# Kernel optimization log

Measured on AMD Instinct MI355X. Metric: run time of the kernel, lower is better.

The kernel has to match this reference:

```python
import jax, jax.numpy as jnp
import numpy as np

ENT_GRID = 16
ENT_DIM = 64
N_RELATION = 5000
EMB_DIM = ENT_GRID * ENT_DIM  # 1024
BATCH = 8192
LN_EPS = 1e-5


def setup_inputs() -> dict:
    key = jax.random.key(0)
    k1, k2, k3, k4 = jax.random.split(key, 4)
    ent_emb = jax.random.normal(k1, (BATCH, EMB_DIM), dtype=jnp.float32)
    proj_ids = jax.random.randint(k2, (BATCH,), 0, N_RELATION, dtype=jnp.int64)
    # xavier_uniform for relation_tran: fan_in = fan_out treated over last two dims
    lim_t = float(np.sqrt(6.0 / (ENT_GRID + ENT_GRID)))
    relation_tran = jax.random.uniform(
        k3, (N_RELATION, ENT_DIM, ENT_GRID, ENT_GRID), jnp.float32, -lim_t, lim_t)
    lim_b = float(np.sqrt(6.0 / (ENT_DIM + ENT_GRID)))
    relation_bias = jax.random.uniform(
        k4, (N_RELATION, ENT_DIM, ENT_GRID), jnp.float32, -lim_b, lim_b)
    ln_weight = jnp.ones((EMB_DIM,), dtype=jnp.float32)
    ln_bias = jnp.zeros((EMB_DIM,), dtype=jnp.float32)
    return {
        "ent_emb": ent_emb,
        "proj_ids": proj_ids,
        "relation_tran": relation_tran,
        "relation_bias": relation_bias,
        "ln_weight": ln_weight,
        "ln_bias": ln_bias,
    }


def _layer_norm(x, w, b, eps=LN_EPS):
    mu = jnp.mean(x, axis=-1, keepdims=True)
    var = jnp.mean(jnp.square(x - mu), axis=-1, keepdims=True)
    return (x - mu) * jax.lax.rsqrt(var + eps) * w + b


def reference(ent_emb, proj_ids, relation_tran, relation_bias, ln_weight, ln_bias):
    B = ent_emb.shape[0]
    # gather per-query relation transform and bias
    rel_tran = relation_tran[proj_ids]  # (B, ent_dim, g, g)
    rel_bias = relation_bias[proj_ids]  # (B, ent_dim, g)
    # distribute: (B, emb_dim) -> (B, ent_dim, ent_grid); torch.chunk+stack == contiguous reshape
    e = ent_emb.reshape(B, ENT_DIM, ENT_GRID)
    # batched small matmul: (g,g) @ (g,) per (batch, ent_dim) block, plus bias
    x = jnp.einsum('bdgh,bdh->bdg', rel_tran, e) + rel_bias
    out = _layer_norm(x.reshape(B, EMB_DIM), ln_weight, ln_bias)
    return out
```

## Files before the change

kernel.cpp:

```cpp
#include <hip/hip_runtime.h>

#define ENT_GRID 16
#define ENT_DIM  64
#define EMB      1024
#define LN_EPS   1e-5f


__global__ void zero_hist_kernel(int* __restrict__ hist, int n) {
    int i = blockIdx.x * blockDim.x + threadIdx.x;
    if (i < n) hist[i] = 0;
}

__global__ void hist_kernel(const int* __restrict__ ids, int* __restrict__ hist, int B) {
    int i = blockIdx.x * blockDim.x + threadIdx.x;
    if (i < B) atomicAdd(&hist[ids[i]], 1);
}

__global__ __launch_bounds__(1024)
void scan_kernel(const int* __restrict__ hist, int* __restrict__ cursor, int n) {
    const int t = threadIdx.x;
    const int ITEMS = (n + 1023) / 1024;
    int vals[8];
    int lsum = 0;
#pragma unroll
    for (int k = 0; k < 8; ++k) {
        int i = t * ITEMS + k;
        int v = (k < ITEMS && i < n) ? hist[i] : 0;
        vals[k] = v;
        lsum += v;
    }
    __shared__ int s[1024];
    s[t] = lsum;
    __syncthreads();
    for (int off = 1; off < 1024; off <<= 1) {
        int v = (t >= off) ? s[t - off] : 0;
        __syncthreads();
        s[t] += v;
        __syncthreads();
    }
    int run = s[t] - lsum;
#pragma unroll
    for (int k = 0; k < 8; ++k) {
        int i = t * ITEMS + k;
        if (k < ITEMS && i < n) cursor[i] = run;
        run += vals[k];
    }
}

__global__ void scatter_kernel(const int* __restrict__ ids, int* __restrict__ cursor,
                               int* __restrict__ perm, int B) {
    int i = blockIdx.x * blockDim.x + threadIdx.x;
    if (i < B) {
        int pos = atomicAdd(&cursor[ids[i]], 1);
        perm[pos] = i;
    }
}

__device__ __forceinline__ float dot4(float4 a, float4 b) {
    return a.x * b.x + a.y * b.y + a.z * b.z + a.w * b.w;
}

__global__ __launch_bounds__(1024, 8)
void wproj_group_kernel(const float* __restrict__ ent_emb,
                        const float* __restrict__ rel_tran,
                        const float* __restrict__ rel_bias,
                        const float* __restrict__ ln_w,
                        const float* __restrict__ ln_b,
                        const int*   __restrict__ hist,
                        const int*   __restrict__ cursor_end,
                        const int*   __restrict__ perm,
                        float* __restrict__ out) {
    const int r   = blockIdx.x;
    const int cnt = hist[r];
    if (cnt == 0) return;
    const int start = cursor_end[r] - cnt;
    const int t = threadIdx.x;
    const int w = t >> 6;

    const float4* __restrict__ tr4 = reinterpret_cast<const float4*>(
        rel_tran + (size_t)r * (ENT_DIM * ENT_GRID * ENT_GRID) + (size_t)t * ENT_GRID);
    const float4 t0 = tr4[0], t1 = tr4[1], t2 = tr4[2], t3 = tr4[3];
    const float bv  = rel_bias[(size_t)r * EMB + t];
    const float lwv = ln_w[t];
    const float lbv = ln_b[t];

    __shared__ __align__(16) float se[2][EMB];
    __shared__ __align__(16) float wred[2][2][16];

    int   bcur = perm[start];
    float vcur = ent_emb[(size_t)bcur * EMB + t];

    for (int j = 0; j < cnt; ++j) {
        const int jb = j & 1;
        se[jb][t] = vcur;

        int bnext = 0; float vnext = 0.0f;
        if (j + 1 < cnt) {
            bnext = perm[start + j + 1];
            vnext = ent_emb[(size_t)bnext * EMB + t];
        }

        asm volatile("s_waitcnt lgkmcnt(0)\n\ts_barrier" ::: "memory");

        const float4* __restrict__ er =
            reinterpret_cast<const float4*>(&se[jb][(t >> 4) * ENT_GRID]);
        const float x = bv + dot4(t0, er[0]) + dot4(t1, er[1])
                           + dot4(t2, er[2]) + dot4(t3, er[3]);

        float s = x, ss = x * x;
#pragma unroll
        for (int off = 32; off > 0; off >>= 1) {
            s  += __shfl_xor(s, off, 64);
            ss += __shfl_xor(ss, off, 64);
        }
        if ((t & 63) == 0) { wred[jb][0][w] = s; wred[jb][1][w] = ss; }

        asm volatile("s_waitcnt lgkmcnt(0)\n\ts_barrier" ::: "memory");

        float tsum = 0.0f, tsq = 0.0f;
        const float4* __restrict__ ps = reinterpret_cast<const float4*>(&wred[jb][0][0]);
        const float4* __restrict__ pq = reinterpret_cast<const float4*>(&wred[jb][1][0]);
#pragma unroll
        for (int q = 0; q < 4; ++q) {
            const float4 a = ps[q];
            const float4 c = pq[q];
            tsum += a.x + a.y + a.z + a.w;
            tsq  += c.x + c.y + c.z + c.w;
        }
        const float mu   = tsum * (1.0f / (float)EMB);
        const float var  = tsq * (1.0f / (float)EMB) - mu * mu;
        const float rstd = rsqrtf(var + LN_EPS);

        out[(size_t)bcur * EMB + t] = (x - mu) * rstd * lwv + lbv;

        bcur = bnext;
        vcur = vnext;
    }
}

extern "C" void kernel_launch(void* const* d_in, const int* in_sizes, int n_in,
                              void* d_out, int out_size, void* d_ws, size_t ws_size,
                              hipStream_t stream) {
    const float* ent_emb  = (const float*)d_in[0];
    const int*   proj_ids = (const int*)  d_in[1];
    const float* rel_tran = (const float*)d_in[2];
    const float* rel_bias = (const float*)d_in[3];
    const float* ln_w     = (const float*)d_in[4];
    const float* ln_b     = (const float*)d_in[5];
    float* out = (float*)d_out;

    const int B  = in_sizes[1];
    const int NR = in_sizes[2] / (ENT_DIM * ENT_GRID * ENT_GRID);

    int* w      = (int*)d_ws;
    int* hist   = w;
    int* cursor = w + NR;
    int* perm   = w + 2 * NR;

    zero_hist_kernel<<<(NR + 255) / 256, 256, 0, stream>>>(hist, NR);
    hist_kernel<<<(B + 255) / 256, 256, 0, stream>>>(proj_ids, hist, B);
    scan_kernel<<<1, 1024, 0, stream>>>(hist, cursor, NR);
    scatter_kernel<<<(B + 255) / 256, 256, 0, stream>>>(proj_ids, cursor, perm, B);

    wproj_group_kernel<<<NR, 1024, 0, stream>>>(ent_emb, rel_tran, rel_bias, ln_w, ln_b,
                                                hist, cursor, perm, out);
}
```

Before: 100.1 us.

## Split relation-grouped projection into quarter blocks and separate LayerNorm pass

The 1024-thread per-relation block becomes four 256-thread blocks, each covering a quarter of the embedding. Each block writes the unnormalized projection plus per-wave partial sums to workspace, and a new per-row kernel then reduces the partials and applies LayerNorm in place. This removes the two block-wide barriers per row and spreads relation work across more, smaller blocks. In exchange the output is written and read an extra time, each quarter reads the entity row from global memory directly, and there is one more launch.

```diff
diff --git a/kernel.cpp b/kernel.cpp
--- a/kernel.cpp
+++ b/kernel.cpp
@@ -60,52 +60,39 @@
     return a.x * b.x + a.y * b.y + a.z * b.z + a.w * b.w;
 }
 
-__global__ __launch_bounds__(1024, 8)
-void wproj_group_kernel(const float* __restrict__ ent_emb,
-                        const float* __restrict__ rel_tran,
-                        const float* __restrict__ rel_bias,
-                        const float* __restrict__ ln_w,
-                        const float* __restrict__ ln_b,
-                        const int*   __restrict__ hist,
-                        const int*   __restrict__ cursor_end,
-                        const int*   __restrict__ perm,
-                        float* __restrict__ out) {
-    const int r   = blockIdx.x;
+__global__ __launch_bounds__(256, 8)
+void wproj_quarter_kernel(const float* __restrict__ ent_emb,
+                          const float* __restrict__ rel_tran,
+                          const float* __restrict__ rel_bias,
+                          const int*   __restrict__ hist,
+                          const int*   __restrict__ cursor_end,
+                          const int*   __restrict__ perm,
+                          float* __restrict__ xout,
+                          float2* __restrict__ part) {
+    const int blk = blockIdx.x;
+    const int r   = blk >> 2;
+    const int q   = blk & 3;
     const int cnt = hist[r];
     if (cnt == 0) return;
     const int start = cursor_end[r] - cnt;
     const int t = threadIdx.x;
     const int w = t >> 6;
+    const int i = q * 256 + t;
+    const int d = i >> 4;
 
     const float4* __restrict__ tr4 = reinterpret_cast<const float4*>(
-        rel_tran + (size_t)r * (ENT_DIM * ENT_GRID * ENT_GRID) + (size_t)t * ENT_GRID);
-    const float4 t0 = tr4[0], t1 = tr4[1], t2 = tr4[2], t3 = tr4[3];
-    const float bv  = rel_bias[(size_t)r * EMB + t];
-    const float lwv = ln_w[t];
-    const float lbv = ln_b[t];
-
-    __shared__ __align__(16) float se[2][EMB];
-    __shared__ __align__(16) float wred[2][2][16];
-
-    int   bcur = perm[start];
-    float vcur = ent_emb[(size_t)bcur * EMB + t];
+        rel_tran + (size_t)r * (ENT_DIM * ENT_GRID * ENT_GRID) + (size_t)i * ENT_GRID);
+    const float4 a0 = tr4[0], a1 = tr4[1], a2 = tr4[2], a3 = tr4[3];
+    const float bv = rel_bias[(size_t)r * EMB + i];
 
     for (int j = 0; j < cnt; ++j) {
-        const int jb = j & 1;
-        se[jb][t] = vcur;
+        const int b = perm[start + j];
+        const float4* __restrict__ e4 =
+            reinterpret_cast<const float4*>(ent_emb + (size_t)b * EMB + d * ENT_GRID);
+        const float4 e0 = e4[0], e1 = e4[1], e2 = e4[2], e3 = e4[3];
 
-        int bnext = 0; float vnext = 0.0f;
-        if (j + 1 < cnt) {
-            bnext = perm[start + j + 1];
-            vnext = ent_emb[(size_t)bnext * EMB + t];
-        }
-
-        asm volatile("s_waitcnt lgkmcnt(0)\n\ts_barrier" ::: "memory");
-
-        const float4* __restrict__ er =
-            reinterpret_cast<const float4*>(&se[jb][(t >> 4) * ENT_GRID]);
-        const float x = bv + dot4(t0, er[0]) + dot4(t1, er[1])
-                           + dot4(t2, er[2]) + dot4(t3, er[3]);
+        const float x = bv + dot4(a0, e0) + dot4(a1, e1) + dot4(a2, e2) + dot4(a3, e3);
+        xout[(size_t)b * EMB + i] = x;
 
         float s = x, ss = x * x;
 #pragma unroll
@@ -113,29 +100,47 @@
             s  += __shfl_xor(s, off, 64);
             ss += __shfl_xor(ss, off, 64);
         }
-        if ((t & 63) == 0) { wred[jb][0][w] = s; wred[jb][1][w] = ss; }
+        if ((t & 63) == 0) part[(size_t)b * 16 + q * 4 + w] = make_float2(s, ss);
+    }
+}
 
-        asm volatile("s_waitcnt lgkmcnt(0)\n\ts_barrier" ::: "memory");
+__global__ __launch_bounds__(256, 8)
+void ln_kernel(const float2* __restrict__ part,
+               const float*  __restrict__ ln_w,
+               const float*  __restrict__ ln_b,
+               float* __restrict__ out) {
+    const int b = blockIdx.x;
+    const int t = threadIdx.x;
+    __shared__ float sstat[2];
 
-        float tsum = 0.0f, tsq = 0.0f;
-        const float4* __restrict__ ps = reinterpret_cast<const float4*>(&wred[jb][0][0]);
-        const float4* __restrict__ pq = reinterpret_cast<const float4*>(&wred[jb][1][0]);
+    if (t < 64) {
+        float s = 0.0f, ss = 0.0f;
+        if (t < 16) { const float2 p = part[(size_t)b * 16 + t]; s = p.x; ss = p.y; }
 #pragma unroll
-        for (int q = 0; q < 4; ++q) {
-            const float4 a = ps[q];
-            const float4 c = pq[q];
-            tsum += a.x + a.y + a.z + a.w;
-            tsq  += c.x + c.y + c.z + c.w;
+        for (int off = 8; off > 0; off >>= 1) {
+            s  += __shfl_xor(s, off, 64);
+            ss += __shfl_xor(ss, off, 64);
         }
-        const float mu   = tsum * (1.0f / (float)EMB);
-        const float var  = tsq * (1.0f / (float)EMB) - mu * mu;
-        const float rstd = rsqrtf(var + LN_EPS);
+        if (t == 0) {
+            const float mu  = s * (1.0f / (float)EMB);
+            const float var = ss * (1.0f / (float)EMB) - mu * mu;
+            sstat[0] = mu;
+            sstat[1] = rsqrtf(var + LN_EPS);
+        }
+    }
+    __syncthreads();
+    const float mu = sstat[0], rstd = sstat[1];
 
-        out[(size_t)bcur * EMB + t] = (x - mu) * rstd * lwv + lbv;
-
-        bcur = bnext;
-        vcur = vnext;
-    }
+    float4* __restrict__ o4 = reinterpret_cast<float4*>(out + (size_t)b * EMB);
+    const float4 x  = o4[t];
+    const float4 w  = reinterpret_cast<const float4*>(ln_w)[t];
+    const float4 bb = reinterpret_cast<const float4*>(ln_b)[t];
+    float4 o;
+    o.x = (x.x - mu) * rstd * w.x + bb.x;
+    o.y = (x.y - mu) * rstd * w.y + bb.y;
+    o.z = (x.z - mu) * rstd * w.z + bb.z;
+    o.w = (x.w - mu) * rstd * w.w + bb.w;
+    o4[t] = o;
 }
 
 extern "C" void kernel_launch(void* const* d_in, const int* in_sizes, int n_in,
@@ -156,12 +161,16 @@
     int* hist   = w;
     int* cursor = w + NR;
     int* perm   = w + 2 * NR;
+    size_t int_bytes = (size_t)(2 * NR + B) * sizeof(int);
+    int_bytes = (int_bytes + 15) & ~(size_t)15;
+    float2* part = (float2*)((char*)d_ws + int_bytes);
 
     zero_hist_kernel<<<(NR + 255) / 256, 256, 0, stream>>>(hist, NR);
     hist_kernel<<<(B + 255) / 256, 256, 0, stream>>>(proj_ids, hist, B);
     scan_kernel<<<1, 1024, 0, stream>>>(hist, cursor, NR);
     scatter_kernel<<<(B + 255) / 256, 256, 0, stream>>>(proj_ids, cursor, perm, B);
 
-    wproj_group_kernel<<<NR, 1024, 0, stream>>>(ent_emb, rel_tran, rel_bias, ln_w, ln_b,
-                                                hist, cursor, perm, out);
+    wproj_quarter_kernel<<<NR * 4, 256, 0, stream>>>(ent_emb, rel_tran, rel_bias,
+                                                     hist, cursor, perm, out, part);
+    ln_kernel<<<B, 256, 0, stream>>>(part, ln_w, ln_b, out);
 }
```

Measured after the change: 99.97 us. About the same (-0.1%).

## Compact nonempty relations into work list and compute four outputs per thread

Applied to the files above, without the earlier changes.

The scan kernel now emits a compacted list of nonempty relations (id, start, count), and the main kernel indexes that list instead of launching per-relation blocks that exit early. The main kernel drops to 256 threads, each holding a full 4x16 transform slice in registers and reading entity vectors directly from global memory as float4, which removes the shared-memory staging and one barrier per row. The zero kernel is replaced by a memset. This cuts empty-block overhead and synchronization, at the cost of much higher register pressure (64 floats of transform per thread) and redundant global reads of entity data across threads.

```diff
diff --git a/kernel.cpp b/kernel.cpp
--- a/kernel.cpp
+++ b/kernel.cpp
@@ -6,18 +6,14 @@
 #define LN_EPS   1e-5f
 
 
-__global__ void zero_hist_kernel(int* __restrict__ hist, int n) {
-    int i = blockIdx.x * blockDim.x + threadIdx.x;
-    if (i < n) hist[i] = 0;
-}
-
 __global__ void hist_kernel(const int* __restrict__ ids, int* __restrict__ hist, int B) {
     int i = blockIdx.x * blockDim.x + threadIdx.x;
     if (i < B) atomicAdd(&hist[ids[i]], 1);
 }
 
 __global__ __launch_bounds__(1024)
-void scan_kernel(const int* __restrict__ hist, int* __restrict__ cursor, int n) {
+void scan_kernel(const int* __restrict__ hist, int* __restrict__ cursor,
+                 int4* __restrict__ work, int* __restrict__ nwork, int n) {
     const int t = threadIdx.x;
     const int ITEMS = (n + 1023) / 1024;
     int vals[8];
@@ -42,7 +38,13 @@
 #pragma unroll
     for (int k = 0; k < 8; ++k) {
         int i = t * ITEMS + k;
-        if (k < ITEMS && i < n) cursor[i] = run;
+        if (k < ITEMS && i < n) {
+            cursor[i] = run;
+            if (vals[k] > 0) {
+                int idx = atomicAdd(nwork, 1);
+                work[idx] = make_int4(i, run, vals[k], 0);
+            }
+        }
         run += vals[k];
     }
 }
@@ -60,81 +62,92 @@
     return a.x * b.x + a.y * b.y + a.z * b.z + a.w * b.w;
 }
 
-__global__ __launch_bounds__(1024, 8)
-void wproj_group_kernel(const float* __restrict__ ent_emb,
+__global__ __launch_bounds__(256, 3)
+void wproj_fused_kernel(const float* __restrict__ ent_emb,
                         const float* __restrict__ rel_tran,
                         const float* __restrict__ rel_bias,
                         const float* __restrict__ ln_w,
                         const float* __restrict__ ln_b,
-                        const int*   __restrict__ hist,
-                        const int*   __restrict__ cursor_end,
+                        const int4*  __restrict__ work,
+                        const int*   __restrict__ nwork,
                         const int*   __restrict__ perm,
                         float* __restrict__ out) {
-    const int r   = blockIdx.x;
-    const int cnt = hist[r];
-    if (cnt == 0) return;
-    const int start = cursor_end[r] - cnt;
-    const int t = threadIdx.x;
-    const int w = t >> 6;
+    const int w = blockIdx.x;
+    if (w >= *nwork) return;
+    const int4 wk   = work[w];
+    const int r     = wk.x;
+    const int start = wk.y;
+    const int cnt   = wk.z;
+    const int t  = threadIdx.x;
+    const int wv = t >> 6;
+    const int d  = t >> 2;
 
     const float4* __restrict__ tr4 = reinterpret_cast<const float4*>(
-        rel_tran + (size_t)r * (ENT_DIM * ENT_GRID * ENT_GRID) + (size_t)t * ENT_GRID);
-    const float4 t0 = tr4[0], t1 = tr4[1], t2 = tr4[2], t3 = tr4[3];
-    const float bv  = rel_bias[(size_t)r * EMB + t];
-    const float lwv = ln_w[t];
-    const float lbv = ln_b[t];
+        rel_tran + (size_t)r * (ENT_DIM * ENT_GRID * ENT_GRID) + (size_t)t * 64);
+    float4 trv[16];
+#pragma unroll
+    for (int m = 0; m < 16; ++m) trv[m] = tr4[m];
+    const float4 bv = reinterpret_cast<const float4*>(rel_bias + (size_t)r * EMB)[t];
+    const float4 lw = reinterpret_cast<const float4*>(ln_w)[t];
+    const float4 lb = reinterpret_cast<const float4*>(ln_b)[t];
 
-    __shared__ __align__(16) float se[2][EMB];
-    __shared__ __align__(16) float wred[2][2][16];
+    __shared__ float2 wred[2][4];
 
-    int   bcur = perm[start];
-    float vcur = ent_emb[(size_t)bcur * EMB + t];
+    const int last = start + cnt - 1;
+    int b0 = perm[start];
+    int b1 = perm[min(start + 1, last)];
+    {
+        const float4* __restrict__ e4 =
+            reinterpret_cast<const float4*>(ent_emb + (size_t)b0 * EMB + d * ENT_GRID);
+        float4 e0 = e4[0], e1 = e4[1], e2 = e4[2], e3 = e4[3];
 
-    for (int j = 0; j < cnt; ++j) {
-        const int jb = j & 1;
-        se[jb][t] = vcur;
+        for (int j = 0; j < cnt; ++j) {
+            const int jb = j & 1;
+            const int bcur = b0;
 
-        int bnext = 0; float vnext = 0.0f;
-        if (j + 1 < cnt) {
-            bnext = perm[start + j + 1];
-            vnext = ent_emb[(size_t)bnext * EMB + t];
+            const int b2 = perm[min(start + j + 2, last)];
+            const float4* __restrict__ n4 =
+                reinterpret_cast<const float4*>(ent_emb + (size_t)b1 * EMB + d * ENT_GRID);
+            const float4 f0 = n4[0], f1 = n4[1], f2 = n4[2], f3 = n4[3];
+
+            const float x0 = bv.x + dot4(trv[ 0], e0) + dot4(trv[ 1], e1)
+                                  + dot4(trv[ 2], e2) + dot4(trv[ 3], e3);
+            const float x1 = bv.y + dot4(trv[ 4], e0) + dot4(trv[ 5], e1)
+                                  + dot4(trv[ 6], e2) + dot4(trv[ 7], e3);
+            const float x2 = bv.z + dot4(trv[ 8], e0) + dot4(trv[ 9], e1)
+                                  + dot4(trv[10], e2) + dot4(trv[11], e3);
+            const float x3 = bv.w + dot4(trv[12], e0) + dot4(trv[13], e1)
+                                  + dot4(trv[14], e2) + dot4(trv[15], e3);
+
+            float s  = x0 + x1 + x2 + x3;
+            float ss = x0 * x0 + x1 * x1 + x2 * x2 + x3 * x3;
+#pragma unroll
+            for (int off = 32; off > 0; off >>= 1) {
+                s  += __shfl_xor(s, off, 64);
+                ss += __shfl_xor(ss, off, 64);
+            }
+            if ((t & 63) == 0) wred[jb][wv] = make_float2(s, ss);
+
+            asm volatile("s_waitcnt lgkmcnt(0)\n\ts_barrier" ::: "memory");
+
+            const float2 p0 = wred[jb][0], p1 = wred[jb][1],
+                         p2 = wred[jb][2], p3 = wred[jb][3];
+            const float ts = p0.x + p1.x + p2.x + p3.x;
+            const float tq = p0.y + p1.y + p2.y + p3.y;
+            const float mu   = ts * (1.0f / (float)EMB);
+            const float var  = tq * (1.0f / (float)EMB) - mu * mu;
+            const float rstd = rsqrtf(var + LN_EPS);
+
+            float4 o;
+            o.x = (x0 - mu) * rstd * lw.x + lb.x;
+            o.y = (x1 - mu) * rstd * lw.y + lb.y;
+            o.z = (x2 - mu) * rstd * lw.z + lb.z;
+            o.w = (x3 - mu) * rstd * lw.w + lb.w;
+            reinterpret_cast<float4*>(out + (size_t)bcur * EMB)[t] = o;
+
+            b0 = b1; b1 = b2;
+            e0 = f0; e1 = f1; e2 = f2; e3 = f3;
         }
-
-        asm volatile("s_waitcnt lgkmcnt(0)\n\ts_barrier" ::: "memory");
-
-        const float4* __restrict__ er =
-            reinterpret_cast<const float4*>(&se[jb][(t >> 4) * ENT_GRID]);
-        const float x = bv + dot4(t0, er[0]) + dot4(t1, er[1])
-                           + dot4(t2, er[2]) + dot4(t3, er[3]);
-
-        float s = x, ss = x * x;
-#pragma unroll
-        for (int off = 32; off > 0; off >>= 1) {
-            s  += __shfl_xor(s, off, 64);
-            ss += __shfl_xor(ss, off, 64);
-        }
-        if ((t & 63) == 0) { wred[jb][0][w] = s; wred[jb][1][w] = ss; }
-
-        asm volatile("s_waitcnt lgkmcnt(0)\n\ts_barrier" ::: "memory");
-
-        float tsum = 0.0f, tsq = 0.0f;
-        const float4* __restrict__ ps = reinterpret_cast<const float4*>(&wred[jb][0][0]);
-        const float4* __restrict__ pq = reinterpret_cast<const float4*>(&wred[jb][1][0]);
-#pragma unroll
-        for (int q = 0; q < 4; ++q) {
-            const float4 a = ps[q];
-            const float4 c = pq[q];
-            tsum += a.x + a.y + a.z + a.w;
-            tsq  += c.x + c.y + c.z + c.w;
-        }
-        const float mu   = tsum * (1.0f / (float)EMB);
-        const float var  = tsq * (1.0f / (float)EMB) - mu * mu;
-        const float rstd = rsqrtf(var + LN_EPS);
-
-        out[(size_t)bcur * EMB + t] = (x - mu) * rstd * lwv + lbv;
-
-        bcur = bnext;
-        vcur = vnext;
     }
 }
 
@@ -152,16 +165,20 @@
     const int B  = in_sizes[1];
     const int NR = in_sizes[2] / (ENT_DIM * ENT_GRID * ENT_GRID);
 
-    int* w      = (int*)d_ws;
-    int* hist   = w;
-    int* cursor = w + NR;
-    int* perm   = w + 2 * NR;
+    int* ws     = (int*)d_ws;
+    int* hist   = ws;
+    int* nwork  = ws + NR;
+    int* cursor = ws + NR + 1;
+    int* perm   = ws + 2 * NR + 1;
+    size_t off = (size_t)(2 * NR + 1 + B) * sizeof(int);
+    off = (off + 15) & ~(size_t)15;
+    int4* work = (int4*)((char*)d_ws + off);
 
-    zero_hist_kernel<<<(NR + 255) / 256, 256, 0, stream>>>(hist, NR);
+    hipMemsetAsync(hist, 0, (size_t)(NR + 1) * sizeof(int), stream);
     hist_kernel<<<(B + 255) / 256, 256, 0, stream>>>(proj_ids, hist, B);
-    scan_kernel<<<1, 1024, 0, stream>>>(hist, cursor, NR);
+    scan_kernel<<<1, 1024, 0, stream>>>(hist, cursor, work, nwork, NR);
     scatter_kernel<<<(B + 255) / 256, 256, 0, stream>>>(proj_ids, cursor, perm, B);
 
-    wproj_group_kernel<<<NR, 1024, 0, stream>>>(ent_emb, rel_tran, rel_bias, ln_w, ln_b,
-                                                hist, cursor, perm, out);
+    wproj_fused_kernel<<<NR, 256, 0, stream>>>(ent_emb, rel_tran, rel_bias, ln_w, ln_b,
+                                               work, nwork, perm, out);
 }
```

Measured after the change: 100.1 us. About the same (+0.1%).
